# Optimization experiments

Measured on AMD Instinct MI355X. Metric: run time of the kernel, lower is better.

## Reference

```python
import jax, jax.numpy as jnp
import numpy as np

HEADS = 8
DIM_HEAD = 64
SCALE = DIM_HEAD ** -0.5

def setup_inputs() -> dict:
    key = jax.random.key(0)
    ks = jax.random.split(key, 6)
    b, n, m, qd, cd = 4, 2048, 2048, 256, 256
    inner = HEADS * DIM_HEAD
    return {
        "x": jax.random.normal(ks[0], (b, n, qd), jnp.float32),
        "context": jax.random.normal(ks[1], (b, m, cd), jnp.float32),
        "Wq": jax.random.normal(ks[2], (inner, qd), jnp.float32) * 0.02,
        "bq": jnp.zeros((inner,), jnp.float32),
        "Wkv": jax.random.normal(ks[3], (2 * inner, cd), jnp.float32) * 0.02,
        "bkv": jnp.zeros((2 * inner,), jnp.float32),
        "Wo": jax.random.normal(ks[4], (qd, inner), jnp.float32) * 0.02,
        "bo": jnp.zeros((qd,), jnp.float32),
    }

def reference(x, context, Wq, bq, Wkv, bkv, Wo, bo):
    b, n, _ = x.shape
    m = context.shape[1]
    inner = HEADS * DIM_HEAD
    # 1x1 conv projections == pointwise linear
    q = jnp.einsum('bnd,ed->bne', x, Wq) + bq            # [b, n, inner]
    kv = jnp.einsum('bmd,ed->bme', context, Wkv) + bkv    # [b, m, 2*inner]
    k, v = kv[..., :inner], kv[..., inner:]
    q = q.reshape(b, n, HEADS, DIM_HEAD).transpose(0, 2, 1, 3)  # [b,h,n,d]
    k = k.reshape(b, m, HEADS, DIM_HEAD).transpose(0, 2, 1, 3)
    v = v.reshape(b, m, HEADS, DIM_HEAD).transpose(0, 2, 1, 3)
    sim = jnp.einsum('bhid,bhjd->bhij', q, k) * SCALE     # [b,h,n,m]
    attn = jax.nn.softmax(sim, axis=-1)
    out = jnp.einsum('bhij,bhjd->bhid', attn, v)          # [b,h,n,d]
    out = out.transpose(0, 2, 1, 3).reshape(b, n, inner)  # [b,n,inner]
    return jnp.einsum('bne,oe->bno', out, Wo) + bo        # [b,n,query_dim]
```

## Files before the change

kernel.cpp:

```cpp
#include <hip/hip_runtime.h>
#include <hip/hip_bf16.h>

#define NB 4
#define SEQ 2048
#define NHEADS 8

typedef __attribute__((ext_vector_type(8))) short bf16x8;
typedef __attribute__((ext_vector_type(4))) short bf16x4;
typedef __attribute__((ext_vector_type(4))) float f32x4;

__device__ inline short f2bf(float x) {
    union { float f; unsigned u; } v; v.f = x;
    unsigned r = v.u + 0x7FFF + ((v.u >> 16) & 1);
    return (short)(r >> 16);
}

__device__ inline unsigned pack2bf(float a, float b) {
    __hip_bfloat162 h = __float22bfloat162_rn(make_float2(a, b));
    unsigned u; __builtin_memcpy(&u, &h, 4);
    return u;
}

__global__ __launch_bounds__(256) void cvt_all(
    const float* __restrict__ x, const float* __restrict__ ctx,
    const float* __restrict__ wq, const float* __restrict__ wkv,
    const float* __restrict__ wo,
    short* __restrict__ xb, short* __restrict__ cb, short* __restrict__ wqb,
    short* __restrict__ wkvb, short* __restrict__ wob)
{
    const int i = blockIdx.x * 256 + threadIdx.x;
    const float* src; short* dst; int off;
    if (i < 524288)       { src = x;   dst = xb;   off = i; }
    else if (i < 1048576) { src = ctx; dst = cb;   off = i - 524288; }
    else if (i < 1081344) { src = wq;  dst = wqb;  off = i - 1048576; }
    else if (i < 1146880) { src = wkv; dst = wkvb; off = i - 1081344; }
    else                  { src = wo;  dst = wob;  off = i - 1146880; }
    const float4 v = ((const float4*)src)[off];
    uint2 o2;
    o2.x = pack2bf(v.x, v.y);
    o2.y = pack2bf(v.z, v.w);
    *(uint2*)(dst + (size_t)off * 4) = o2;
}

template <bool OUT_BF16>
__global__ __launch_bounds__(256) void gemm_bf16(
    const short* __restrict__ A,
    const short* __restrict__ W,
    const float* __restrict__ bias,
    void* __restrict__ out,
    int K, int Ccols, float scale)
{
    __shared__ short As[128 * 64];
    __shared__ short Ws[128 * 64];
    const int tid = threadIdx.x;
    const int w = tid >> 6;
    const int lane = tid & 63;
    const int low = lane & 15;
    const int quad = lane >> 4;
    const int wm = w >> 1;
    const int wn = w & 1;
    const int rM0 = blockIdx.y * 128;
    const int c0 = blockIdx.x * 128;

    const int srow = tid >> 3;
    const int sj = tid & 7;

    f32x4 acc[4][4];
#pragma unroll
    for (int mt = 0; mt < 4; ++mt)
#pragma unroll
        for (int nt = 0; nt < 4; ++nt) acc[mt][nt] = (f32x4){0.f, 0.f, 0.f, 0.f};

    bf16x8 pa[4], pwr[4];
#pragma unroll
    for (int c = 0; c < 4; ++c) {
        const int row = c * 32 + srow;
        pa[c]  = *(const bf16x8*)(A + (size_t)(rM0 + row) * K + sj * 8);
        pwr[c] = *(const bf16x8*)(W + (size_t)(c0 + row) * K + sj * 8);
    }

    int k0 = 0;
    for (;;) {
        __syncthreads();
#pragma unroll
        for (int c = 0; c < 4; ++c) {
            const int row = c * 32 + srow;
            const int pc = sj ^ (row & 7);
            *(bf16x8*)(&As[row * 64 + pc * 8]) = pa[c];
            *(bf16x8*)(&Ws[row * 64 + pc * 8]) = pwr[c];
        }
        __syncthreads();
        const int kn = k0 + 64;
        if (kn < K) {
#pragma unroll
            for (int c = 0; c < 4; ++c) {
                const int row = c * 32 + srow;
                pa[c]  = *(const bf16x8*)(A + (size_t)(rM0 + row) * K + kn + sj * 8);
                pwr[c] = *(const bf16x8*)(W + (size_t)(c0 + row) * K + kn + sj * 8);
            }
        }
#pragma unroll
        for (int kh = 0; kh < 2; ++kh) {
            bf16x8 af[4], bfv[4];
#pragma unroll
            for (int t = 0; t < 4; ++t) {
                const int ra = wm * 64 + t * 16 + low;
                af[t] = *(const bf16x8*)(&As[ra * 64 + ((kh * 4 + quad) ^ (ra & 7)) * 8]);
                const int rb = wn * 64 + t * 16 + low;
                bfv[t] = *(const bf16x8*)(&Ws[rb * 64 + ((kh * 4 + quad) ^ (rb & 7)) * 8]);
            }
#pragma unroll
            for (int mt = 0; mt < 4; ++mt)
#pragma unroll
                for (int nt = 0; nt < 4; ++nt)
                    acc[mt][nt] = __builtin_amdgcn_mfma_f32_16x16x32_bf16(af[mt], bfv[nt], acc[mt][nt], 0, 0, 0);
        }
        k0 = kn;
        if (k0 >= K) break;
    }

#pragma unroll
    for (int nt = 0; nt < 4; ++nt) {
        const int col = c0 + wn * 64 + nt * 16 + low;
        const float bv = bias[col];
#pragma unroll
        for (int mt = 0; mt < 4; ++mt) {
            const size_t rbase = (size_t)(rM0 + wm * 64 + mt * 16 + quad * 4);
#pragma unroll
            for (int r = 0; r < 4; ++r) {
                const float val = (acc[mt][nt][r] + bv) * scale;
                if (OUT_BF16) ((short*)out)[(rbase + r) * Ccols + col] = f2bf(val);
                else          ((float*)out)[(rbase + r) * Ccols + col] = val;
            }
        }
    }
}

#define KST 72
#define VST 72
#define PST 72

__global__ __launch_bounds__(256) void attn_mfma(
    const short* __restrict__ q2,
    const short* __restrict__ kv2,
    short* __restrict__ o)
{
    __shared__ short Ks[64 * KST];
    __shared__ short Vt[64 * VST];
    __shared__ short Ps[4][32 * PST];

    const int tid = threadIdx.x;
    const int w = tid >> 6;
    const int lane = tid & 63;
    const int low = lane & 15;
    const int quad = lane >> 4;

    const int bh = blockIdx.y;
    const int b = bh >> 3;
    const int h = bh & 7;
    const int iq0 = blockIdx.x * 128;

    bf16x8 qf[2][2];
#pragma unroll
    for (int qt = 0; qt < 2; ++qt)
#pragma unroll
        for (int kh = 0; kh < 2; ++kh)
            qf[qt][kh] = *(const bf16x8*)(q2 + (size_t)(b * SEQ + iq0 + w * 32 + qt * 16 + low) * 512
                                          + h * 64 + kh * 32 + quad * 8);

    const short* kbase = kv2 + (size_t)(b * SEQ) * 1024 + h * 64;
    const short* vbase = kbase + 512;
    short* pw = &Ps[w][0];

    float lsum[2][4];
#pragma unroll
    for (int qt = 0; qt < 2; ++qt)
#pragma unroll
        for (int r = 0; r < 4; ++r) lsum[qt][r] = 0.f;
    f32x4 oacc[2][4];
#pragma unroll
    for (int qt = 0; qt < 2; ++qt)
#pragma unroll
        for (int dt = 0; dt < 4; ++dt) oacc[qt][dt] = (f32x4){0.f, 0.f, 0.f, 0.f};

    const int krow = tid >> 2;
    const int kc = (tid & 3) * 16;
    const int vk4 = (tid & 15) * 4;
    const int vd4 = (tid >> 4) * 4;

    bf16x8 pk0, pk1;
    bf16x4 pv0, pv1, pv2, pv3;
    {
        const short* ksrc = kbase + (size_t)krow * 1024 + kc;
        pk0 = *(const bf16x8*)(ksrc);
        pk1 = *(const bf16x8*)(ksrc + 8);
        const short* vs = vbase + (size_t)vk4 * 1024 + vd4;
        pv0 = *(const bf16x4*)(vs);
        pv1 = *(const bf16x4*)(vs + 1024);
        pv2 = *(const bf16x4*)(vs + 2048);
        pv3 = *(const bf16x4*)(vs + 3072);
    }

    for (int jt = 0; jt < SEQ / 64; ++jt) {
        __syncthreads();
        *(bf16x8*)(&Ks[krow * KST + kc]) = pk0;
        *(bf16x8*)(&Ks[krow * KST + kc + 8]) = pk1;
        {
            bf16x4 c0_, c1_, c2_, c3_;
            c0_[0] = pv0[0]; c0_[1] = pv1[0]; c0_[2] = pv2[0]; c0_[3] = pv3[0];
            c1_[0] = pv0[1]; c1_[1] = pv1[1]; c1_[2] = pv2[1]; c1_[3] = pv3[1];
            c2_[0] = pv0[2]; c2_[1] = pv1[2]; c2_[2] = pv2[2]; c2_[3] = pv3[2];
            c3_[0] = pv0[3]; c3_[1] = pv1[3]; c3_[2] = pv2[3]; c3_[3] = pv3[3];
            *(bf16x4*)(&Vt[(vd4 + 0) * VST + vk4]) = c0_;
            *(bf16x4*)(&Vt[(vd4 + 1) * VST + vk4]) = c1_;
            *(bf16x4*)(&Vt[(vd4 + 2) * VST + vk4]) = c2_;
            *(bf16x4*)(&Vt[(vd4 + 3) * VST + vk4]) = c3_;
        }
        __syncthreads();

        if (jt + 1 < SEQ / 64) {
            const short* ksrc = kbase + (size_t)((jt + 1) * 64 + krow) * 1024 + kc;
            pk0 = *(const bf16x8*)(ksrc);
            pk1 = *(const bf16x8*)(ksrc + 8);
            const short* vs = vbase + (size_t)((jt + 1) * 64 + vk4) * 1024 + vd4;
            pv0 = *(const bf16x4*)(vs);
            pv1 = *(const bf16x4*)(vs + 1024);
            pv2 = *(const bf16x4*)(vs + 2048);
            pv3 = *(const bf16x4*)(vs + 3072);
        }

#pragma unroll
        for (int nt = 0; nt < 4; ++nt) {
            const bf16x8 kb0 = *(const bf16x8*)(&Ks[(nt * 16 + low) * KST + quad * 8]);
            const bf16x8 kb1 = *(const bf16x8*)(&Ks[(nt * 16 + low) * KST + 32 + quad * 8]);
#pragma unroll
            for (int qt = 0; qt < 2; ++qt) {
                f32x4 s = (f32x4){0.f, 0.f, 0.f, 0.f};
                s = __builtin_amdgcn_mfma_f32_16x16x32_bf16(qf[qt][0], kb0, s, 0, 0, 0);
                s = __builtin_amdgcn_mfma_f32_16x16x32_bf16(qf[qt][1], kb1, s, 0, 0, 0);
                const float p0 = __builtin_amdgcn_exp2f(s[0]);
                const float p1 = __builtin_amdgcn_exp2f(s[1]);
                const float p2 = __builtin_amdgcn_exp2f(s[2]);
                const float p3 = __builtin_amdgcn_exp2f(s[3]);
                lsum[qt][0] += p0; lsum[qt][1] += p1;
                lsum[qt][2] += p2; lsum[qt][3] += p3;
                const unsigned u01 = pack2bf(p0, p1);
                const unsigned u23 = pack2bf(p2, p3);
                short* pb = &pw[(qt * 16 + quad * 4) * PST + nt * 16 + low];
                pb[0]       = (short)(u01 & 0xffff);
                pb[PST]     = (short)(u01 >> 16);
                pb[2 * PST] = (short)(u23 & 0xffff);
                pb[3 * PST] = (short)(u23 >> 16);
            }
        }
        __builtin_amdgcn_wave_barrier();

#pragma unroll
        for (int kb = 0; kb < 2; ++kb) {
            bf16x8 pfr[2];
#pragma unroll
            for (int qt = 0; qt < 2; ++qt)
                pfr[qt] = *(const bf16x8*)(&pw[(qt * 16 + low) * PST + kb * 32 + quad * 8]);
#pragma unroll
            for (int dt = 0; dt < 4; ++dt) {
                const bf16x8 vf = *(const bf16x8*)(&Vt[(dt * 16 + low) * VST + kb * 32 + quad * 8]);
                oacc[0][dt] = __builtin_amdgcn_mfma_f32_16x16x32_bf16(pfr[0], vf, oacc[0][dt], 0, 0, 0);
                oacc[1][dt] = __builtin_amdgcn_mfma_f32_16x16x32_bf16(pfr[1], vf, oacc[1][dt], 0, 0, 0);
            }
        }
        __builtin_amdgcn_wave_barrier();
    }

#pragma unroll
    for (int qt = 0; qt < 2; ++qt) {
        float linv[4];
#pragma unroll
        for (int r = 0; r < 4; ++r) {
            float x = lsum[qt][r];
            x += __shfl_xor(x, 1);
            x += __shfl_xor(x, 2);
            x += __shfl_xor(x, 4);
            x += __shfl_xor(x, 8);
            linv[r] = 1.f / x;
        }
        short* obase = o + (size_t)(b * SEQ + iq0 + w * 32 + qt * 16 + quad * 4) * 512 + h * 64;
#pragma unroll
        for (int r = 0; r < 4; ++r)
#pragma unroll
            for (int dt = 0; dt < 4; ++dt)
                obase[(size_t)r * 512 + dt * 16 + low] = f2bf(oacc[qt][dt][r] * linv[r]);
    }
}

extern "C" void kernel_launch(void* const* d_in, const int* in_sizes, int n_in,
                              void* d_out, int out_size, void* d_ws, size_t ws_size,
                              hipStream_t stream) {
    const float* x   = (const float*)d_in[0];
    const float* ctx = (const float*)d_in[1];
    const float* Wq  = (const float*)d_in[2];
    const float* bq  = (const float*)d_in[3];
    const float* Wkv = (const float*)d_in[4];
    const float* bkv = (const float*)d_in[5];
    const float* Wo  = (const float*)d_in[6];
    const float* bo  = (const float*)d_in[7];
    float* out = (float*)d_out;

    const int ROWS = NB * SEQ;
    short* xb   = (short*)d_ws;
    short* cb   = xb + 2097152;
    short* wqb  = cb + 2097152;
    short* wkvb = wqb + 131072;
    short* wob  = wkvb + 262144;
    short* q2b  = wob + 131072;
    short* kv2b = q2b + (size_t)ROWS * 512;
    short* owsb = kv2b + (size_t)ROWS * 1024;

    cvt_all<<<4608, 256, 0, stream>>>(x, ctx, Wq, Wkv, Wo, xb, cb, wqb, wkvb, wob);

    const float qscale = 0.125f * 1.44269504088896f;
    gemm_bf16<true><<<dim3(512 / 128, ROWS / 128), 256, 0, stream>>>(
        xb, wqb, bq, q2b, 256, 512, qscale);
    gemm_bf16<true><<<dim3(1024 / 128, ROWS / 128), 256, 0, stream>>>(
        cb, wkvb, bkv, kv2b, 256, 1024, 1.0f);
    attn_mfma<<<dim3(SEQ / 128, NB * NHEADS), 256, 0, stream>>>(q2b, kv2b, owsb);
    gemm_bf16<false><<<dim3(256 / 128, ROWS / 128), 256, 0, stream>>>(
        owsb, wob, bo, out, 512, 256, 1.0f);
}
```

Baseline: 170.1 us.

## Fuse all stages into one persistent kernel with grid-wide atomic barriers

Replaces the five separate launches (convert, Q GEMM, KV GEMM, attention, output GEMM) with one persistent 512-block kernel that moves between phases through a software grid barrier on an atomic counter. The GEMM tiles shrink to 64x64 so enough tiles exist to share across the fixed grid, and the attention row-sum is reduced once at the end instead of per element. This removes launch gaps and tail effects between stages, at the cost of barrier spin overhead, smaller and less efficient GEMM tiles, and a deadlock risk if all 512 blocks cannot be resident at once.

```diff
diff --git a/kernel.cpp b/kernel.cpp
--- a/kernel.cpp
+++ b/kernel.cpp
@@ -1,13 +1,24 @@
 #include <hip/hip_runtime.h>
 #include <hip/hip_bf16.h>
 
-#define NB 4
 #define SEQ 2048
 #define NHEADS 8
+#define ROWS 8192
+#define NBLK 512
 
 typedef __attribute__((ext_vector_type(8))) short bf16x8;
 typedef __attribute__((ext_vector_type(4))) short bf16x4;
 typedef __attribute__((ext_vector_type(4))) float f32x4;
+
+#define XB_OFF   0u
+#define CB_OFF   (XB_OFF + ROWS * 256)
+#define WQ_OFF   (CB_OFF + ROWS * 256)
+#define WKV_OFF  (WQ_OFF + 512 * 256)
+#define WO_OFF   (WKV_OFF + 1024 * 256)
+#define Q2_OFF   (WO_OFF + 256 * 512)
+#define KV_OFF   (Q2_OFF + (size_t)ROWS * 512)
+#define OB_OFF   (KV_OFF + (size_t)ROWS * 1024)
+#define CNT_BYTES ((size_t)(OB_OFF + (size_t)ROWS * 512) * 2)
 
 __device__ inline short f2bf(float x) {
     union { float f; unsigned u; } v; v.f = x;
@@ -21,98 +32,74 @@
     return u;
 }
 
-__global__ __launch_bounds__(256) void cvt_all(
-    const float* __restrict__ x, const float* __restrict__ ctx,
-    const float* __restrict__ wq, const float* __restrict__ wkv,
-    const float* __restrict__ wo,
-    short* __restrict__ xb, short* __restrict__ cb, short* __restrict__ wqb,
-    short* __restrict__ wkvb, short* __restrict__ wob)
+__device__ inline void gbar(unsigned* cnt, unsigned target) {
+    __syncthreads();
+    __threadfence();
+    if (threadIdx.x == 0) {
+        atomicAdd(cnt, 1u);
+        while (atomicAdd(cnt, 0u) < target) __builtin_amdgcn_s_sleep(8);
+    }
+    __syncthreads();
+    __threadfence();
+}
+
+template <bool OUT_BF16>
+__device__ __forceinline__ void gemm_tile(
+    const short* __restrict__ A, const short* __restrict__ W,
+    const float* __restrict__ bias, void* __restrict__ outp,
+    int K, int Ccols, float scale, int r0, int c0,
+    short* As, short* Ws, int tid)
 {
-    const int i = blockIdx.x * 256 + threadIdx.x;
-    const float* src; short* dst; int off;
-    if (i < 524288)       { src = x;   dst = xb;   off = i; }
-    else if (i < 1048576) { src = ctx; dst = cb;   off = i - 524288; }
-    else if (i < 1081344) { src = wq;  dst = wqb;  off = i - 1048576; }
-    else if (i < 1146880) { src = wkv; dst = wkvb; off = i - 1081344; }
-    else                  { src = wo;  dst = wob;  off = i - 1146880; }
-    const float4 v = ((const float4*)src)[off];
-    uint2 o2;
-    o2.x = pack2bf(v.x, v.y);
-    o2.y = pack2bf(v.z, v.w);
-    *(uint2*)(dst + (size_t)off * 4) = o2;
-}
-
-template <bool OUT_BF16>
-__global__ __launch_bounds__(256) void gemm_bf16(
-    const short* __restrict__ A,
-    const short* __restrict__ W,
-    const float* __restrict__ bias,
-    void* __restrict__ out,
-    int K, int Ccols, float scale)
-{
-    __shared__ short As[128 * 64];
-    __shared__ short Ws[128 * 64];
-    const int tid = threadIdx.x;
-    const int w = tid >> 6;
-    const int lane = tid & 63;
-    const int low = lane & 15;
-    const int quad = lane >> 4;
-    const int wm = w >> 1;
-    const int wn = w & 1;
-    const int rM0 = blockIdx.y * 128;
-    const int c0 = blockIdx.x * 128;
-
-    const int srow = tid >> 3;
-    const int sj = tid & 7;
-
-    f32x4 acc[4][4];
-#pragma unroll
-    for (int mt = 0; mt < 4; ++mt)
-#pragma unroll
-        for (int nt = 0; nt < 4; ++nt) acc[mt][nt] = (f32x4){0.f, 0.f, 0.f, 0.f};
-
-    bf16x8 pa[4], pwr[4];
-#pragma unroll
-    for (int c = 0; c < 4; ++c) {
-        const int row = c * 32 + srow;
-        pa[c]  = *(const bf16x8*)(A + (size_t)(rM0 + row) * K + sj * 8);
-        pwr[c] = *(const bf16x8*)(W + (size_t)(c0 + row) * K + sj * 8);
+    const int w = tid >> 6, lane = tid & 63, low = lane & 15, quad = lane >> 4;
+    const int wm = w >> 1, wn = w & 1;
+    const int srow = tid >> 2;
+    const int sc = (tid & 3) * 2;
+
+    f32x4 acc[2][2];
+#pragma unroll
+    for (int mt = 0; mt < 2; ++mt)
+#pragma unroll
+        for (int nt = 0; nt < 2; ++nt) acc[mt][nt] = (f32x4){0.f, 0.f, 0.f, 0.f};
+
+    bf16x8 pab[2], pwb[2];
+    {
+        const short* ap = A + (size_t)(r0 + srow) * K + sc * 8;
+        const short* wp = W + (size_t)(c0 + srow) * K + sc * 8;
+        pab[0] = ((const bf16x8*)ap)[0]; pab[1] = ((const bf16x8*)ap)[1];
+        pwb[0] = ((const bf16x8*)wp)[0]; pwb[1] = ((const bf16x8*)wp)[1];
     }
 
     int k0 = 0;
     for (;;) {
         __syncthreads();
 #pragma unroll
-        for (int c = 0; c < 4; ++c) {
-            const int row = c * 32 + srow;
-            const int pc = sj ^ (row & 7);
-            *(bf16x8*)(&As[row * 64 + pc * 8]) = pa[c];
-            *(bf16x8*)(&Ws[row * 64 + pc * 8]) = pwr[c];
+        for (int c = 0; c < 2; ++c) {
+            const int pc = (sc + c) ^ (srow & 7);
+            *(bf16x8*)(&As[srow * 64 + pc * 8]) = pab[c];
+            *(bf16x8*)(&Ws[srow * 64 + pc * 8]) = pwb[c];
         }
         __syncthreads();
         const int kn = k0 + 64;
         if (kn < K) {
-#pragma unroll
-            for (int c = 0; c < 4; ++c) {
-                const int row = c * 32 + srow;
-                pa[c]  = *(const bf16x8*)(A + (size_t)(rM0 + row) * K + kn + sj * 8);
-                pwr[c] = *(const bf16x8*)(W + (size_t)(c0 + row) * K + kn + sj * 8);
-            }
+            const short* ap = A + (size_t)(r0 + srow) * K + kn + sc * 8;
+            const short* wp = W + (size_t)(c0 + srow) * K + kn + sc * 8;
+            pab[0] = ((const bf16x8*)ap)[0]; pab[1] = ((const bf16x8*)ap)[1];
+            pwb[0] = ((const bf16x8*)wp)[0]; pwb[1] = ((const bf16x8*)wp)[1];
         }
 #pragma unroll
         for (int kh = 0; kh < 2; ++kh) {
-            bf16x8 af[4], bfv[4];
-#pragma unroll
-            for (int t = 0; t < 4; ++t) {
-                const int ra = wm * 64 + t * 16 + low;
+            bf16x8 af[2], bfv[2];
+#pragma unroll
+            for (int t = 0; t < 2; ++t) {
+                const int ra = wm * 32 + t * 16 + low;
                 af[t] = *(const bf16x8*)(&As[ra * 64 + ((kh * 4 + quad) ^ (ra & 7)) * 8]);
-                const int rb = wn * 64 + t * 16 + low;
+                const int rb = wn * 32 + t * 16 + low;
                 bfv[t] = *(const bf16x8*)(&Ws[rb * 64 + ((kh * 4 + quad) ^ (rb & 7)) * 8]);
             }
 #pragma unroll
-            for (int mt = 0; mt < 4; ++mt)
-#pragma unroll
-                for (int nt = 0; nt < 4; ++nt)
+            for (int mt = 0; mt < 2; ++mt)
+#pragma unroll
+                for (int nt = 0; nt < 2; ++nt)
                     acc[mt][nt] = __builtin_amdgcn_mfma_f32_16x16x32_bf16(af[mt], bfv[nt], acc[mt][nt], 0, 0, 0);
         }
         k0 = kn;
@@ -120,17 +107,17 @@
     }
 
 #pragma unroll
-    for (int nt = 0; nt < 4; ++nt) {
-        const int col = c0 + wn * 64 + nt * 16 + low;
+    for (int nt = 0; nt < 2; ++nt) {
+        const int col = c0 + wn * 32 + nt * 16 + low;
         const float bv = bias[col];
 #pragma unroll
-        for (int mt = 0; mt < 4; ++mt) {
-            const size_t rbase = (size_t)(rM0 + wm * 64 + mt * 16 + quad * 4);
+        for (int mt = 0; mt < 2; ++mt) {
+            const size_t rbase = (size_t)(r0 + wm * 32 + mt * 16 + quad * 4);
 #pragma unroll
             for (int r = 0; r < 4; ++r) {
                 const float val = (acc[mt][nt][r] + bv) * scale;
-                if (OUT_BF16) ((short*)out)[(rbase + r) * Ccols + col] = f2bf(val);
-                else          ((float*)out)[(rbase + r) * Ccols + col] = val;
+                if (OUT_BF16) ((short*)outp)[(rbase + r) * Ccols + col] = f2bf(val);
+                else          ((float*)outp)[(rbase + r) * Ccols + col] = val;
             }
         }
     }
@@ -140,155 +127,201 @@
 #define VST 72
 #define PST 72
 
-__global__ __launch_bounds__(256) void attn_mfma(
-    const short* __restrict__ q2,
-    const short* __restrict__ kv2,
-    short* __restrict__ o)
+__global__ __launch_bounds__(256, 2) void fused_all(
+    const float* __restrict__ x, const float* __restrict__ ctx,
+    const float* __restrict__ Wq, const float* __restrict__ bq,
+    const float* __restrict__ Wkv, const float* __restrict__ bkv,
+    const float* __restrict__ Wo, const float* __restrict__ bo,
+    float* __restrict__ out, short* __restrict__ ws, unsigned* __restrict__ cnt)
 {
-    __shared__ short Ks[64 * KST];
-    __shared__ short Vt[64 * VST];
-    __shared__ short Ps[4][32 * PST];
-
+    __shared__ short smem[18432];
     const int tid = threadIdx.x;
-    const int w = tid >> 6;
-    const int lane = tid & 63;
-    const int low = lane & 15;
-    const int quad = lane >> 4;
-
-    const int bh = blockIdx.y;
-    const int b = bh >> 3;
-    const int h = bh & 7;
-    const int iq0 = blockIdx.x * 128;
-
-    bf16x8 qf[2][2];
-#pragma unroll
-    for (int qt = 0; qt < 2; ++qt)
-#pragma unroll
-        for (int kh = 0; kh < 2; ++kh)
-            qf[qt][kh] = *(const bf16x8*)(q2 + (size_t)(b * SEQ + iq0 + w * 32 + qt * 16 + low) * 512
-                                          + h * 64 + kh * 32 + quad * 8);
-
-    const short* kbase = kv2 + (size_t)(b * SEQ) * 1024 + h * 64;
-    const short* vbase = kbase + 512;
-    short* pw = &Ps[w][0];
-
-    float lsum[2][4];
-#pragma unroll
-    for (int qt = 0; qt < 2; ++qt)
-#pragma unroll
-        for (int r = 0; r < 4; ++r) lsum[qt][r] = 0.f;
-    f32x4 oacc[2][4];
-#pragma unroll
-    for (int qt = 0; qt < 2; ++qt)
-#pragma unroll
-        for (int dt = 0; dt < 4; ++dt) oacc[qt][dt] = (f32x4){0.f, 0.f, 0.f, 0.f};
-
-    const int krow = tid >> 2;
-    const int kc = (tid & 3) * 16;
-    const int vk4 = (tid & 15) * 4;
-    const int vd4 = (tid >> 4) * 4;
-
-    bf16x8 pk0, pk1;
-    bf16x4 pv0, pv1, pv2, pv3;
-    {
-        const short* ksrc = kbase + (size_t)krow * 1024 + kc;
-        pk0 = *(const bf16x8*)(ksrc);
-        pk1 = *(const bf16x8*)(ksrc + 8);
-        const short* vs = vbase + (size_t)vk4 * 1024 + vd4;
-        pv0 = *(const bf16x4*)(vs);
-        pv1 = *(const bf16x4*)(vs + 1024);
-        pv2 = *(const bf16x4*)(vs + 2048);
-        pv3 = *(const bf16x4*)(vs + 3072);
-    }
-
-    for (int jt = 0; jt < SEQ / 64; ++jt) {
-        __syncthreads();
-        *(bf16x8*)(&Ks[krow * KST + kc]) = pk0;
-        *(bf16x8*)(&Ks[krow * KST + kc + 8]) = pk1;
+    const int bid = blockIdx.x;
+
+    short* xb   = ws + XB_OFF;
+    short* cb   = ws + CB_OFF;
+    short* wqb  = ws + WQ_OFF;
+    short* wkvb = ws + WKV_OFF;
+    short* wob  = ws + WO_OFF;
+    short* q2b  = ws + Q2_OFF;
+    short* kv2b = ws + KV_OFF;
+    short* ob   = ws + OB_OFF;
+
+    {
+        int i = bid * 256 + tid;
+#pragma unroll
+        for (int it = 0; it < 9; ++it, i += NBLK * 256) {
+            const float* src; short* dst; int off;
+            if (i < 524288)       { src = x;   dst = xb;   off = i; }
+            else if (i < 1048576) { src = ctx; dst = cb;   off = i - 524288; }
+            else if (i < 1081344) { src = Wq;  dst = wqb;  off = i - 1048576; }
+            else if (i < 1146880) { src = Wkv; dst = wkvb; off = i - 1081344; }
+            else                  { src = Wo;  dst = wob;  off = i - 1146880; }
+            const float4 v = ((const float4*)src)[off];
+            uint2 o2;
+            o2.x = pack2bf(v.x, v.y);
+            o2.y = pack2bf(v.z, v.w);
+            *(uint2*)(dst + (size_t)off * 4) = o2;
+        }
+    }
+    gbar(cnt, NBLK);
+
+    {
+        const float qscale = 0.125f * 1.44269504088896f;
+        short* As = smem;
+        short* Ws = smem + 8192;
+#pragma unroll 1
+        for (int u = bid; u < 1024; u += NBLK)
+            gemm_tile<true>(xb, wqb, bq, q2b, 256, 512, qscale,
+                            (u >> 3) * 64, (u & 7) * 64, As, Ws, tid);
+#pragma unroll 1
+        for (int u = bid; u < 2048; u += NBLK)
+            gemm_tile<true>(cb, wkvb, bkv, kv2b, 256, 1024, 1.0f,
+                            (u >> 4) * 64, (u & 15) * 64, As, Ws, tid);
+    }
+    gbar(cnt, 2 * NBLK);
+
+    {
+        short* Ks = smem;
+        short* Vt = smem + 4608;
+        const int w = tid >> 6;
+        const int lane = tid & 63;
+        const int low = lane & 15;
+        const int quad = lane >> 4;
+        short* pw = smem + 9216 + w * (32 * PST);
+
+        const int h = bid & 7;
+        const int rest = bid >> 3;
+        const int qtile = rest & 15;
+        const int b = rest >> 4;
+        const int iq0 = qtile * 128;
+
+        bf16x8 qf[2][2];
+#pragma unroll
+        for (int qt = 0; qt < 2; ++qt)
+#pragma unroll
+            for (int kh = 0; kh < 2; ++kh)
+                qf[qt][kh] = *(const bf16x8*)(q2b + (size_t)(b * SEQ + iq0 + w * 32 + qt * 16 + low) * 512
+                                              + h * 64 + kh * 32 + quad * 8);
+
+        const short* kbase = kv2b + (size_t)(b * SEQ) * 1024 + h * 64;
+        const short* vbase = kbase + 512;
+
+        float lsum[2] = {0.f, 0.f};
+        f32x4 oacc[2][4];
+#pragma unroll
+        for (int qt = 0; qt < 2; ++qt)
+#pragma unroll
+            for (int dt = 0; dt < 4; ++dt) oacc[qt][dt] = (f32x4){0.f, 0.f, 0.f, 0.f};
+
+        const int krow = tid >> 2;
+        const int kc = (tid & 3) * 16;
+        const int vk4 = (tid & 15) * 4;
+        const int vd4 = (tid >> 4) * 4;
+
+        bf16x8 pk0, pk1;
+        bf16x4 pv0, pv1, pv2, pv3;
         {
-            bf16x4 c0_, c1_, c2_, c3_;
-            c0_[0] = pv0[0]; c0_[1] = pv1[0]; c0_[2] = pv2[0]; c0_[3] = pv3[0];
-            c1_[0] = pv0[1]; c1_[1] = pv1[1]; c1_[2] = pv2[1]; c1_[3] = pv3[1];
-            c2_[0] = pv0[2]; c2_[1] = pv1[2]; c2_[2] = pv2[2]; c2_[3] = pv3[2];
-            c3_[0] = pv0[3]; c3_[1] = pv1[3]; c3_[2] = pv2[3]; c3_[3] = pv3[3];
-            *(bf16x4*)(&Vt[(vd4 + 0) * VST + vk4]) = c0_;
-            *(bf16x4*)(&Vt[(vd4 + 1) * VST + vk4]) = c1_;
-            *(bf16x4*)(&Vt[(vd4 + 2) * VST + vk4]) = c2_;
-            *(bf16x4*)(&Vt[(vd4 + 3) * VST + vk4]) = c3_;
-        }
-        __syncthreads();
-
-        if (jt + 1 < SEQ / 64) {
-            const short* ksrc = kbase + (size_t)((jt + 1) * 64 + krow) * 1024 + kc;
+            const short* ksrc = kbase + (size_t)krow * 1024 + kc;
             pk0 = *(const bf16x8*)(ksrc);
             pk1 = *(const bf16x8*)(ksrc + 8);
-            const short* vs = vbase + (size_t)((jt + 1) * 64 + vk4) * 1024 + vd4;
+            const short* vs = vbase + (size_t)vk4 * 1024 + vd4;
             pv0 = *(const bf16x4*)(vs);
             pv1 = *(const bf16x4*)(vs + 1024);
             pv2 = *(const bf16x4*)(vs + 2048);
             pv3 = *(const bf16x4*)(vs + 3072);
         }
 
-#pragma unroll
-        for (int nt = 0; nt < 4; ++nt) {
-            const bf16x8 kb0 = *(const bf16x8*)(&Ks[(nt * 16 + low) * KST + quad * 8]);
-            const bf16x8 kb1 = *(const bf16x8*)(&Ks[(nt * 16 + low) * KST + 32 + quad * 8]);
-#pragma unroll
-            for (int qt = 0; qt < 2; ++qt) {
-                f32x4 s = (f32x4){0.f, 0.f, 0.f, 0.f};
-                s = __builtin_amdgcn_mfma_f32_16x16x32_bf16(qf[qt][0], kb0, s, 0, 0, 0);
-                s = __builtin_amdgcn_mfma_f32_16x16x32_bf16(qf[qt][1], kb1, s, 0, 0, 0);
-                const float p0 = __builtin_amdgcn_exp2f(s[0]);
-                const float p1 = __builtin_amdgcn_exp2f(s[1]);
-                const float p2 = __builtin_amdgcn_exp2f(s[2]);
-                const float p3 = __builtin_amdgcn_exp2f(s[3]);
-                lsum[qt][0] += p0; lsum[qt][1] += p1;
-                lsum[qt][2] += p2; lsum[qt][3] += p3;
-                const unsigned u01 = pack2bf(p0, p1);
-                const unsigned u23 = pack2bf(p2, p3);
-                short* pb = &pw[(qt * 16 + quad * 4) * PST + nt * 16 + low];
-                pb[0]       = (short)(u01 & 0xffff);
-                pb[PST]     = (short)(u01 >> 16);
-                pb[2 * PST] = (short)(u23 & 0xffff);
-                pb[3 * PST] = (short)(u23 >> 16);
-            }
-        }
-        __builtin_amdgcn_wave_barrier();
-
-#pragma unroll
-        for (int kb = 0; kb < 2; ++kb) {
-            bf16x8 pfr[2];
-#pragma unroll
-            for (int qt = 0; qt < 2; ++qt)
-                pfr[qt] = *(const bf16x8*)(&pw[(qt * 16 + low) * PST + kb * 32 + quad * 8]);
-#pragma unroll
-            for (int dt = 0; dt < 4; ++dt) {
-                const bf16x8 vf = *(const bf16x8*)(&Vt[(dt * 16 + low) * VST + kb * 32 + quad * 8]);
-                oacc[0][dt] = __builtin_amdgcn_mfma_f32_16x16x32_bf16(pfr[0], vf, oacc[0][dt], 0, 0, 0);
-                oacc[1][dt] = __builtin_amdgcn_mfma_f32_16x16x32_bf16(pfr[1], vf, oacc[1][dt], 0, 0, 0);
-            }
-        }
-        __builtin_amdgcn_wave_barrier();
-    }
-
-#pragma unroll
-    for (int qt = 0; qt < 2; ++qt) {
-        float linv[4];
-#pragma unroll
-        for (int r = 0; r < 4; ++r) {
-            float x = lsum[qt][r];
-            x += __shfl_xor(x, 1);
-            x += __shfl_xor(x, 2);
-            x += __shfl_xor(x, 4);
-            x += __shfl_xor(x, 8);
-            linv[r] = 1.f / x;
-        }
-        short* obase = o + (size_t)(b * SEQ + iq0 + w * 32 + qt * 16 + quad * 4) * 512 + h * 64;
-#pragma unroll
-        for (int r = 0; r < 4; ++r)
-#pragma unroll
-            for (int dt = 0; dt < 4; ++dt)
-                obase[(size_t)r * 512 + dt * 16 + low] = f2bf(oacc[qt][dt][r] * linv[r]);
+        for (int jt = 0; jt < SEQ / 64; ++jt) {
+            __syncthreads();
+            *(bf16x8*)(&Ks[krow * KST + kc]) = pk0;
+            *(bf16x8*)(&Ks[krow * KST + kc + 8]) = pk1;
+            {
+                bf16x4 c0_, c1_, c2_, c3_;
+                c0_[0] = pv0[0]; c0_[1] = pv1[0]; c0_[2] = pv2[0]; c0_[3] = pv3[0];
+                c1_[0] = pv0[1]; c1_[1] = pv1[1]; c1_[2] = pv2[1]; c1_[3] = pv3[1];
+                c2_[0] = pv0[2]; c2_[1] = pv1[2]; c2_[2] = pv2[2]; c2_[3] = pv3[2];
+                c3_[0] = pv0[3]; c3_[1] = pv1[3]; c3_[2] = pv2[3]; c3_[3] = pv3[3];
+                *(bf16x4*)(&Vt[(vd4 + 0) * VST + vk4]) = c0_;
+                *(bf16x4*)(&Vt[(vd4 + 1) * VST + vk4]) = c1_;
+                *(bf16x4*)(&Vt[(vd4 + 2) * VST + vk4]) = c2_;
+                *(bf16x4*)(&Vt[(vd4 + 3) * VST + vk4]) = c3_;
+            }
+            __syncthreads();
+
+            if (jt + 1 < SEQ / 64) {
+                const short* ksrc = kbase + (size_t)((jt + 1) * 64 + krow) * 1024 + kc;
+                pk0 = *(const bf16x8*)(ksrc);
+                pk1 = *(const bf16x8*)(ksrc + 8);
+                const short* vs = vbase + (size_t)((jt + 1) * 64 + vk4) * 1024 + vd4;
+                pv0 = *(const bf16x4*)(vs);
+                pv1 = *(const bf16x4*)(vs + 1024);
+                pv2 = *(const bf16x4*)(vs + 2048);
+                pv3 = *(const bf16x4*)(vs + 3072);
+            }
+
+#pragma unroll
+            for (int nt = 0; nt < 4; ++nt) {
+                const bf16x8 kf0 = *(const bf16x8*)(&Ks[(nt * 16 + low) * KST + quad * 8]);
+                const bf16x8 kf1 = *(const bf16x8*)(&Ks[(nt * 16 + low) * KST + 32 + quad * 8]);
+#pragma unroll
+                for (int qt = 0; qt < 2; ++qt) {
+                    f32x4 s = (f32x4){0.f, 0.f, 0.f, 0.f};
+                    s = __builtin_amdgcn_mfma_f32_16x16x32_bf16(kf0, qf[qt][0], s, 0, 0, 0);
+                    s = __builtin_amdgcn_mfma_f32_16x16x32_bf16(kf1, qf[qt][1], s, 0, 0, 0);
+                    const float p0 = __builtin_amdgcn_exp2f(s[0]);
+                    const float p1 = __builtin_amdgcn_exp2f(s[1]);
+                    const float p2 = __builtin_amdgcn_exp2f(s[2]);
+                    const float p3 = __builtin_amdgcn_exp2f(s[3]);
+                    lsum[qt] += (p0 + p1) + (p2 + p3);
+                    uint2 u;
+                    u.x = pack2bf(p0, p1);
+                    u.y = pack2bf(p2, p3);
+                    *(uint2*)(&pw[(qt * 16 + low) * PST + nt * 16 + quad * 4]) = u;
+                }
+            }
+            __builtin_amdgcn_wave_barrier();
+
+#pragma unroll
+            for (int kb = 0; kb < 2; ++kb) {
+                bf16x8 pfr[2];
+#pragma unroll
+                for (int qt = 0; qt < 2; ++qt)
+                    pfr[qt] = *(const bf16x8*)(&pw[(qt * 16 + low) * PST + kb * 32 + quad * 8]);
+#pragma unroll
+                for (int dt = 0; dt < 4; ++dt) {
+                    const bf16x8 vf = *(const bf16x8*)(&Vt[(dt * 16 + low) * VST + kb * 32 + quad * 8]);
+                    oacc[0][dt] = __builtin_amdgcn_mfma_f32_16x16x32_bf16(pfr[0], vf, oacc[0][dt], 0, 0, 0);
+                    oacc[1][dt] = __builtin_amdgcn_mfma_f32_16x16x32_bf16(pfr[1], vf, oacc[1][dt], 0, 0, 0);
+                }
+            }
+            __builtin_amdgcn_wave_barrier();
+        }
+
+#pragma unroll
+        for (int qt = 0; qt < 2; ++qt) {
+            float lv = lsum[qt];
+            lv += __shfl_xor(lv, 16);
+            lv += __shfl_xor(lv, 32);
+            float linv[4];
+#pragma unroll
+            for (int r = 0; r < 4; ++r)
+                linv[r] = 1.f / __shfl(lv, quad * 4 + r);
+            short* obase = ob + (size_t)(b * SEQ + iq0 + w * 32 + qt * 16 + quad * 4) * 512 + h * 64;
+#pragma unroll
+            for (int r = 0; r < 4; ++r)
+#pragma unroll
+                for (int dt = 0; dt < 4; ++dt)
+                    obase[(size_t)r * 512 + dt * 16 + low] = f2bf(oacc[qt][dt][r] * linv[r]);
+        }
+    }
+    gbar(cnt, 3 * NBLK);
+
+    {
+        short* As = smem;
+        short* Ws = smem + 8192;
+        gemm_tile<false>(ob, wob, bo, out, 512, 256, 1.0f,
+                         (bid >> 2) * 64, (bid & 3) * 64, As, Ws, tid);
     }
 }
 
@@ -305,24 +338,8 @@
     const float* bo  = (const float*)d_in[7];
     float* out = (float*)d_out;
 
-    const int ROWS = NB * SEQ;
-    short* xb   = (short*)d_ws;
-    short* cb   = xb + 2097152;
-    short* wqb  = cb + 2097152;
-    short* wkvb = wqb + 131072;
-    short* wob  = wkvb + 262144;
-    short* q2b  = wob + 131072;
-    short* kv2b = q2b + (size_t)ROWS * 512;
-    short* owsb = kv2b + (size_t)ROWS * 1024;
-
-    cvt_all<<<4608, 256, 0, stream>>>(x, ctx, Wq, Wkv, Wo, xb, cb, wqb, wkvb, wob);
-
-    const float qscale = 0.125f * 1.44269504088896f;
-    gemm_bf16<true><<<dim3(512 / 128, ROWS / 128), 256, 0, stream>>>(
-        xb, wqb, bq, q2b, 256, 512, qscale);
-    gemm_bf16<true><<<dim3(1024 / 128, ROWS / 128), 256, 0, stream>>>(
-        cb, wkvb, bkv, kv2b, 256, 1024, 1.0f);
-    attn_mfma<<<dim3(SEQ / 128, NB * NHEADS), 256, 0, stream>>>(q2b, kv2b, owsb);
-    gemm_bf16<false><<<dim3(256 / 128, ROWS / 128), 256, 0, stream>>>(
-        owsb, wob, bo, out, 512, 256, 1.0f);
-}
+    unsigned* cnt = (unsigned*)((char*)d_ws + CNT_BYTES);
+    hipMemsetAsync(cnt, 0, sizeof(unsigned), stream);
+    fused_all<<<NBLK, 256, 0, stream>>>(
+        x, ctx, Wq, bq, Wkv, bkv, Wo, bo, out, (short*)d_ws, cnt);
+}
```

Measured after the change: 497.7 us. 193% more time.
